# Kernel optimization log

Measured on AMD Instinct MI355X. Metric: run time of the kernel, lower is better.

## Reference

```python
import jax, jax.numpy as jnp
import numpy as np

B, LATENT, U_DIM, NUM_PROD, NUM_INJ, HID = 4096, 128, 24, 16, 8, 200
ZU = LATENT + U_DIM  # 152


def setup_inputs() -> dict:
    key = jax.random.key(0)
    ks = jax.random.split(key, 24)

    def w(k, shape, fan_in):
        return jax.random.normal(k, shape, jnp.float32) * (1.0 / np.sqrt(fan_in))

    inp = {
        "zt": jax.random.normal(ks[0], (B, LATENT), jnp.float32),
        "dt": jax.random.uniform(ks[1], (B, 1), jnp.float32),
        "ut": jax.random.uniform(ks[2], (B, U_DIM), jnp.float32),
        # trans_encoder: (latent+1) -> 200 -> 200 -> latent, ReLU between
        "We1": w(ks[3], (HID, LATENT + 1), LATENT + 1), "be1": jnp.zeros((HID,), jnp.float32),
        "We2": w(ks[4], (HID, HID), HID),               "be2": jnp.zeros((HID,), jnp.float32),
        "We3": w(ks[5], (LATENT, HID), HID),            "be3": jnp.zeros((LATENT,), jnp.float32),
        # At / Bt projections
        "WA": w(ks[6], (LATENT * LATENT, LATENT), LATENT), "bA": jnp.zeros((LATENT * LATENT,), jnp.float32),
        "WB": w(ks[7], (LATENT * U_DIM, LATENT), LATENT),  "bB": jnp.zeros((LATENT * U_DIM,), jnp.float32),
        # per-well heads, stacked over head dim h: zu(152) -> 64 -> 64 -> 2
        "Wh1": w(ks[8], (NUM_PROD, 64, ZU), ZU),  "bh1": jnp.zeros((NUM_PROD, 64), jnp.float32),
        "Wh2": w(ks[9], (NUM_PROD, 64, 64), 64),  "bh2": jnp.zeros((NUM_PROD, 64), jnp.float32),
        "Wh3": w(ks[10], (NUM_PROD, 2, 64), 64),  "bh3": jnp.zeros((NUM_PROD, 2), jnp.float32),
        # injector head: zu -> num_inj
        "Wi": w(ks[11], (NUM_INJ, ZU), ZU), "bi": jnp.zeros((NUM_INJ,), jnp.float32),
    }
    return inp


def _forward(zt, dt, ut, We1, be1, We2, be2, We3, be3, WA, bA, WB, bB,
             Wh1, bh1, Wh2, bh2, Wh3, bh3, Wi, bi):
    b = zt.shape[0]
    # encoder on [zt, dt]
    x = jnp.concatenate([zt, dt], axis=-1)                      # [B, latent+1]
    h = jax.nn.relu(x @ We1.T + be1)
    h = jax.nn.relu(h @ We2.T + be2)
    hz = h @ We3.T + be3                                        # [B, latent]
    # state transition matrices
    At = (hz @ WA.T + bA).reshape(b, LATENT, LATENT)            # [B, L, L]
    Bt = (hz @ WB.T + bB).reshape(b, LATENT, U_DIM)             # [B, L, U]
    ut_dt = ut * dt                                             # [B, U]
    zt1 = jnp.einsum('bij,bj->bi', At, zt) + jnp.einsum('biu,bu->bi', Bt, ut_dt)
    # per-well heads on zu, fused as batched GEMMs over head dim h
    zu = jnp.concatenate([zt1, ut], axis=-1)                    # [B, 152]
    g = jax.nn.relu(jnp.einsum('bz,hoz->bho', zu, Wh1) + bh1)   # [B, H, 64]
    g = jax.nn.relu(jnp.einsum('bho,hpo->bhp', g, Wh2) + bh2)   # [B, H, 64]
    wells = (jnp.einsum('bho,hpo->bhp', g, Wh3) + bh3).reshape(b, NUM_PROD * 2)
    inj = zu @ Wi.T + bi                                        # [B, num_inj]
    yt1 = jnp.concatenate([wells, inj], axis=-1)                # [B, 40]
    return zt1, yt1


def reference(zt, dt, ut, We1, be1, We2, be2, We3, be3, WA, bA, WB, bB,
              Wh1, bh1, Wh2, bh2, Wh3, bh3, Wi, bi):
    return _forward(zt, dt, ut, We1, be1, We2, be2, We3, be3, WA, bA, WB, bB,
                    Wh1, bh1, Wh2, bh2, Wh3, bh3, Wi, bi)
```

## Files before the change

### kernel.cpp

```cpp
#include <hip/hip_runtime.h>
#include <hip/hip_bf16.h>


#define NB   4096
#define LAT  128
#define UD   24
#define HIDN 200
#define ZUD  152
#define JPD  152

#define GT_OFF      0u
#define GB_OFF      2490368u
#define HZ_OFF      2509824u
#define PART_OFF    3034112u
#define PART_STRIDE 524288u
#define WH1P_OFF    7228416u
#define WH2P_OFF    7392256u
#define WH3P_OFF    7457792u

typedef __attribute__((ext_vector_type(8))) short short8_t;
typedef __attribute__((ext_vector_type(4))) float f32x4;

union FragU { short8_t s; unsigned short u[8]; };
union Frag2 { short8_t s; __hip_bfloat162 h2[4]; };

__device__ __forceinline__ unsigned short bf16_rne(float x) {
  const unsigned u = __float_as_uint(x);
  return (unsigned short)((u + 0x7FFFu + ((u >> 16) & 1u)) >> 16);
}
__device__ __forceinline__ unsigned short bf16_hi(float x) {
  return (unsigned short)(__float_as_uint(x) >> 16);
}
__device__ __forceinline__ unsigned short bf16_lo(float x) {
  const float hif = __uint_as_float(__float_as_uint(x) & 0xFFFF0000u);
  return bf16_rne(x - hif);
}

#define MFMA_BF16(A, B, C) __builtin_amdgcn_mfma_f32_16x16x32_bf16((A), (B), (C), 0, 0, 0)

__global__ __launch_bounds__(256, 5)
void prep_kernel(const float* __restrict__ WA, const float* __restrict__ bA,
                 const float* __restrict__ WB, const float* __restrict__ bB,
                 unsigned short* __restrict__ GtU, float* __restrict__ Gb,
                 const float* __restrict__ zt, const float* __restrict__ dt,
                 const float* __restrict__ We1, const float* __restrict__ be1,
                 const float* __restrict__ We2, const float* __restrict__ be2,
                 const float* __restrict__ We3, const float* __restrict__ be3,
                 float* __restrict__ hz,
                 const float* __restrict__ Wh1, const float* __restrict__ Wh2,
                 const float* __restrict__ Wh3,
                 short8_t* __restrict__ WH1P, short8_t* __restrict__ WH2P,
                 short8_t* __restrict__ WH3P) {
  __shared__ union {
    float tile32[32][132];
    struct { float xs[8][132]; float h1[8][200]; float h2[8][200]; } e;
  } sh;
  const int t = threadIdx.x;

  if (blockIdx.x < 152) {
    const int jp = blockIdx.x;
    const bool isA = (jp < LAT);
    const float* __restrict__ src = isA ? WA : WB;
    const int mul = isA ? LAT : UD;
    const int sub = isA ? jp : (jp - LAT);
    short8_t* __restrict__ G8 = (short8_t*)GtU;

    if (t < 128) {
      const float* __restrict__ bsrc = isA ? bA : bB;
      Gb[(jp << 7) + t] = bsrc[t * mul + sub];
    }

    for (int p = 0; p < 4; ++p) {
      for (int idx = t; idx < 1024; idx += 256) {
        const int i = idx >> 5, c4 = (idx & 31) << 2;
        *(float4*)(&sh.tile32[i][c4]) =
            *(const float4*)(src + (size_t)(((p << 5) + i) * mul + sub) * 128 + c4);
      }
      __syncthreads();
#pragma unroll
      for (int q = 0; q < 4; ++q) {
        const int cc  = (q << 8) + t;
        const int l   = cc & 63;
        const int spl = (cc >> 6) & 1;
        const int nloc = (cc >> 7) & 1;
        const int ksq  = (cc >> 8) & 3;
        const int n    = (p << 1) + nloc;
        const int icl  = (nloc << 4) + (l & 15);
        const int k0   = (ksq << 5) + ((l >> 4) << 3);
        FragU fr;
#pragma unroll
        for (int j = 0; j < 8; ++j) {
          const float g = sh.tile32[icl][k0 + j];
          fr.u[j] = spl ? bf16_lo(g) : bf16_hi(g);
        }
        const int c = ((((ksq << 3) + n) << 1) + spl) * 64 + l;
        G8[(size_t)jp * 4096 + c] = fr.s;
      }
      __syncthreads();
    }
    return;
  }

  if (blockIdx.x >= 664) {
    const int h = blockIdx.x - 664;
    for (int c = t; c < 2560; c += 256) {
      const int l = c & 63, spl = (c >> 6) & 1, nt = (c >> 7) & 3, ks = c >> 9;
      const int col = (nt << 4) + (l & 15);
      const int k0  = (ks << 5) + ((l >> 4) << 3);
      const float* __restrict__ wr = Wh1 + ((size_t)h * 64 + col) * ZUD;
      FragU fr;
#pragma unroll
      for (int j = 0; j < 8; ++j) {
        const int k = k0 + j;
        const float v = (k < ZUD) ? wr[k] : 0.f;
        fr.u[j] = spl ? bf16_lo(v) : bf16_hi(v);
      }
      WH1P[(size_t)h * 2560 + c] = fr.s;
    }
    for (int c = t; c < 1024; c += 256) {
      const int l = c & 63, spl = (c >> 6) & 1, nt = (c >> 7) & 3, ks = (c >> 9) & 1;
      const int col = (nt << 4) + (l & 15);
      const int k0  = (ks << 5) + ((l >> 4) << 3);
      const float* __restrict__ wr = Wh2 + ((size_t)h * 64 + col) * 64 + k0;
      FragU fr;
#pragma unroll
      for (int j = 0; j < 8; ++j) {
        const float v = wr[j];
        fr.u[j] = spl ? bf16_lo(v) : bf16_hi(v);
      }
      WH2P[(size_t)h * 1024 + c] = fr.s;
    }
    for (int c = t; c < 256; c += 256) {
      const int l = c & 63, spl = (c >> 6) & 1, ks = (c >> 7) & 1;
      const int col = l & 15;
      const int k0  = (ks << 5) + ((l >> 4) << 3);
      FragU fr;
#pragma unroll
      for (int j = 0; j < 8; ++j) {
        const float v = (col < 2) ? Wh3[((size_t)h * 2 + col) * 64 + k0 + j] : 0.f;
        fr.u[j] = spl ? bf16_lo(v) : bf16_hi(v);
      }
      WH3P[(size_t)h * 256 + c] = fr.s;
    }
    return;
  }

  const int b0 = (blockIdx.x - 152) * 8;

  for (int idx = t; idx < 8 * 129; idx += 256) {
    const int r = idx / 129, c = idx - r * 129;
    sh.e.xs[r][c] = (c < LAT) ? zt[(size_t)(b0 + r) * LAT + c] : dt[b0 + r];
  }
  __syncthreads();

  if (t < HIDN) {
    const float* __restrict__ w = We1 + t * 129;
    float acc[8];
    const float bias = be1[t];
#pragma unroll
    for (int r = 0; r < 8; ++r) acc[r] = bias;
    for (int c = 0; c < 128; c += 4) {
      const float w0 = w[c], w1 = w[c + 1], w2 = w[c + 2], w3 = w[c + 3];
#pragma unroll
      for (int r = 0; r < 8; ++r) {
        const float4 xv = *(const float4*)(&sh.e.xs[r][c]);
        acc[r] += xv.x * w0 + xv.y * w1 + xv.z * w2 + xv.w * w3;
      }
    }
    const float wl = w[128];
#pragma unroll
    for (int r = 0; r < 8; ++r) sh.e.h1[r][t] = fmaxf(fmaf(sh.e.xs[r][128], wl, acc[r]), 0.f);
  }
  __syncthreads();

  if (t < HIDN) {
    const float* __restrict__ w = We2 + t * HIDN;
    float acc[8];
    const float bias = be2[t];
#pragma unroll
    for (int r = 0; r < 8; ++r) acc[r] = bias;
    for (int c = 0; c < HIDN; c += 4) {
      const float4 wv = *(const float4*)(w + c);
#pragma unroll
      for (int r = 0; r < 8; ++r) {
        const float4 hv = *(const float4*)(&sh.e.h1[r][c]);
        acc[r] += hv.x * wv.x + hv.y * wv.y + hv.z * wv.z + hv.w * wv.w;
      }
    }
#pragma unroll
    for (int r = 0; r < 8; ++r) sh.e.h2[r][t] = fmaxf(acc[r], 0.f);
  }
  __syncthreads();

  if (t < LAT) {
    const float* __restrict__ w = We3 + t * HIDN;
    float acc[8];
    const float bias = be3[t];
#pragma unroll
    for (int r = 0; r < 8; ++r) acc[r] = bias;
    for (int c = 0; c < HIDN; c += 4) {
      const float4 wv = *(const float4*)(w + c);
#pragma unroll
      for (int r = 0; r < 8; ++r) {
        const float4 hv = *(const float4*)(&sh.e.h2[r][c]);
        acc[r] += hv.x * wv.x + hv.y * wv.y + hv.z * wv.z + hv.w * wv.w;
      }
    }
#pragma unroll
    for (int r = 0; r < 8; ++r) hz[(size_t)(b0 + r) * LAT + t] = acc[r];
  }
}

#define GBODY(JP, B00, B01, B10, B11, NJP)                                      \
  {                                                                             \
    const int jp_ = (JP);                                                       \
    const float w0_ = wtile[(rw << 5) + lr][jp_];                               \
    const float w1_ = wtile[(rw << 5) + 16 + lr][jp_];                          \
    Frag2 p0_, p1_;                                                             \
    _Pragma("unroll")                                                           \
    for (int jq = 0; jq < 4; ++jq) {                                            \
      p0_.h2[jq] = __float22bfloat162_rn(                                       \
          make_float2(w0_ * hzr0[2 * jq], w0_ * hzr0[2 * jq + 1]));             \
      p1_.h2[jq] = __float22bfloat162_rn(                                       \
          make_float2(w1_ * hzr1[2 * jq], w1_ * hzr1[2 * jq + 1]));             \
    }                                                                           \
    acc00 = MFMA_BF16(p0_.s, B00, acc00);                                       \
    acc00 = MFMA_BF16(p0_.s, B01, acc00);                                       \
    acc01 = MFMA_BF16(p0_.s, B10, acc01);                                       \
    acc01 = MFMA_BF16(p0_.s, B11, acc01);                                       \
    acc10 = MFMA_BF16(p1_.s, B00, acc10);                                       \
    acc10 = MFMA_BF16(p1_.s, B01, acc10);                                       \
    acc11 = MFMA_BF16(p1_.s, B10, acc11);                                       \
    acc11 = MFMA_BF16(p1_.s, B11, acc11);                                       \
    const size_t nb_ = (size_t)(NJP) * 4096;                                    \
    B00 = G8[nb_ + c00]; B01 = G8[nb_ + c01];                                   \
    B10 = G8[nb_ + c10]; B11 = G8[nb_ + c11];                                   \
  }

__global__ __launch_bounds__(512, 4)
void gemm_mfma_kernel(const float* __restrict__ zt, const float* __restrict__ dt,
                      const float* __restrict__ ut,
                      const unsigned short* __restrict__ GtU,
                      const float* __restrict__ Gb,
                      const float* __restrict__ hz, float* __restrict__ part) {
  __shared__ float wtile[64][156];
  const int t  = threadIdx.x;
  const int l  = t & 63;
  const int w  = t >> 6;
  const int rw = w & 1, cw = w >> 1;
  const int bid   = blockIdx.x;
  const int combo = bid & 7;
  const int ks    = combo & 3;
  const int jph   = combo >> 2;
  const int b0    = (bid >> 3) << 6;
  const int lr  = l & 15, lg = l >> 4;
  const int j0  = jph * 76;

  for (int idx = t; idx < 2048; idx += 512) {
    const int r = idx >> 5, c4 = (idx & 31) << 2;
    *(float4*)(&wtile[r][c4]) = *(const float4*)(zt + (((size_t)(b0 + r)) << 7) + c4);
  }
  for (int idx = t; idx < 384; idx += 512) {
    const int r = idx / 6, u4 = (idx - r * 6) << 2;
    float4 v = *(const float4*)(ut + (size_t)(b0 + r) * UD + u4);
    const float s = dt[b0 + r];
    v.x *= s; v.y *= s; v.z *= s; v.w *= s;
    *(float4*)(&wtile[r][LAT + u4]) = v;
  }
  __syncthreads();

  const int kk = (ks << 5) + (lg << 3);
  float hzr0[8], hzr1[8];
  {
    const float* __restrict__ hp0 = hz + (((size_t)(b0 + (rw << 5) + lr)) << 7) + kk;
    const float* __restrict__ hp1 = hz + (((size_t)(b0 + (rw << 5) + 16 + lr)) << 7) + kk;
    const float4 a0 = *(const float4*)hp0, b0v = *(const float4*)(hp0 + 4);
    const float4 a1 = *(const float4*)hp1, b1v = *(const float4*)(hp1 + 4);
    hzr0[0]=a0.x; hzr0[1]=a0.y; hzr0[2]=a0.z; hzr0[3]=a0.w;
    hzr0[4]=b0v.x; hzr0[5]=b0v.y; hzr0[6]=b0v.z; hzr0[7]=b0v.w;
    hzr1[0]=a1.x; hzr1[1]=a1.y; hzr1[2]=a1.z; hzr1[3]=a1.w;
    hzr1[4]=b1v.x; hzr1[5]=b1v.y; hzr1[6]=b1v.z; hzr1[7]=b1v.w;
  }

  const short8_t* __restrict__ G8 = (const short8_t*)GtU;
  const int n0 = (cw << 1), n1 = (cw << 1) + 1;
  const int c00 = ((((ks << 3) + n0) << 1) + 0) * 64 + l;
  const int c01 = ((((ks << 3) + n0) << 1) + 1) * 64 + l;
  const int c10 = ((((ks << 3) + n1) << 1) + 0) * 64 + l;
  const int c11 = ((((ks << 3) + n1) << 1) + 1) * 64 + l;

  f32x4 acc00 = {0.f,0.f,0.f,0.f}, acc01 = {0.f,0.f,0.f,0.f};
  f32x4 acc10 = {0.f,0.f,0.f,0.f}, acc11 = {0.f,0.f,0.f,0.f};

  short8_t A0 = G8[(size_t)(j0+0)*4096 + c00], A1 = G8[(size_t)(j0+0)*4096 + c01],
           A2 = G8[(size_t)(j0+0)*4096 + c10], A3 = G8[(size_t)(j0+0)*4096 + c11];
  short8_t Bv0 = G8[(size_t)(j0+1)*4096 + c00], Bv1 = G8[(size_t)(j0+1)*4096 + c01],
           Bv2 = G8[(size_t)(j0+1)*4096 + c10], Bv3 = G8[(size_t)(j0+1)*4096 + c11];
  short8_t C0 = G8[(size_t)(j0+2)*4096 + c00], C1 = G8[(size_t)(j0+2)*4096 + c01],
           C2 = G8[(size_t)(j0+2)*4096 + c10], C3 = G8[(size_t)(j0+2)*4096 + c11];
  short8_t D0 = G8[(size_t)(j0+3)*4096 + c00], D1 = G8[(size_t)(j0+3)*4096 + c01],
           D2 = G8[(size_t)(j0+3)*4096 + c10], D3 = G8[(size_t)(j0+3)*4096 + c11];

  const int jend = j0 + 76;
  for (int jp = j0; jp < jend; jp += 4) {
    const int n4 = (jp + 4 < jend) ? jp + 4 : jend - 1;
    const int n5 = (jp + 5 < jend) ? jp + 5 : jend - 1;
    const int n6 = (jp + 6 < jend) ? jp + 6 : jend - 1;
    const int n7 = (jp + 7 < jend) ? jp + 7 : jend - 1;
    GBODY(jp + 0, A0, A1, A2, A3, n4);
    GBODY(jp + 1, Bv0, Bv1, Bv2, Bv3, n5);
    GBODY(jp + 2, C0, C1, C2, C3, n6);
    GBODY(jp + 3, D0, D1, D2, D3, n7);
  }

  {
    const int jb0 = combo * 19;
    for (int jp = jb0; jp < jb0 + 19; ++jp) {
      const float gb0 = Gb[(jp << 7) + (cw << 5) + lr];
      const float gb1 = Gb[(jp << 7) + (cw << 5) + 16 + lr];
#pragma unroll
      for (int r = 0; r < 4; ++r) {
        const float wv0 = wtile[(rw << 5) + (lg << 2) + r][jp];
        const float wv1 = wtile[(rw << 5) + 16 + (lg << 2) + r][jp];
        acc00[r] += wv0 * gb0; acc01[r] += wv0 * gb1;
        acc10[r] += wv1 * gb0; acc11[r] += wv1 * gb1;
      }
    }
  }

  float* __restrict__ dst = part + (size_t)combo * PART_STRIDE + (((size_t)b0) << 7);
  const int colb = (cw << 5) + lr;
#pragma unroll
  for (int r = 0; r < 4; ++r) {
    const int row0 = (rw << 5) + (lg << 2) + r;
    const int row1 = row0 + 16;
    dst[((size_t)row0 << 7) + colb]      = acc00[r];
    dst[((size_t)row0 << 7) + colb + 16] = acc01[r];
    dst[((size_t)row1 << 7) + colb]      = acc10[r];
    dst[((size_t)row1 << 7) + colb + 16] = acc11[r];
  }
}

__global__ __launch_bounds__(512, 4)
void heads_kernel(const float* __restrict__ ut, const float* __restrict__ part,
                  const short8_t* __restrict__ WH1P, const float* __restrict__ bh1,
                  const short8_t* __restrict__ WH2P, const float* __restrict__ bh2,
                  const short8_t* __restrict__ WH3P, const float* __restrict__ bh3,
                  const float* __restrict__ Wi, const float* __restrict__ bi,
                  float* __restrict__ out) {
  __shared__ float    zuf[64][156];
  __shared__ short8_t g1a[1024];
  __shared__ short8_t g2a[1024];
  const int t  = threadIdx.x;
  const int l  = t & 63;
  const int w  = t >> 6;
  const int wm = w >> 1, wn = w & 1;
  const int mb = blockIdx.x >> 2;
  const int hg = blockIdx.x & 3;
  const int b0 = mb << 6;
  float* __restrict__ zt1_out = out;
  float* __restrict__ yt1_out = out + (size_t)NB * LAT;

  for (int idx = t; idx < 2048; idx += 512) {
    const int r = idx >> 5, c4 = (idx & 31) << 2;
    const size_t off = (((size_t)(b0 + r)) << 7) + c4;
    float4 s = *(const float4*)(part + off);
#pragma unroll
    for (int q = 1; q < 8; ++q) {
      const float4 v = *(const float4*)(part + (size_t)q * PART_STRIDE + off);
      s.x += v.x; s.y += v.y; s.z += v.z; s.w += v.w;
    }
    *(float4*)(&zuf[r][c4]) = s;
    if (hg == 0) *(float4*)(zt1_out + off) = s;
  }
  for (int idx = t; idx < 384; idx += 512) {
    const int r = idx / 6, u4 = (idx - r * 6) << 2;
    *(float4*)(&zuf[r][LAT + u4]) = *(const float4*)(ut + (size_t)(b0 + r) * UD + u4);
  }
  __syncthreads();

  short8_t Ahi[5], Alo[5];
  {
    const int arow = (wm << 4) + (l & 15);
#pragma unroll
    for (int ks = 0; ks < 5; ++ks) {
      const int k0 = (ks << 5) + ((l >> 4) << 3);
      FragU fh, fl;
      if (k0 < ZUD) {
        const float4 va = *(const float4*)(&zuf[arow][k0]);
        const float4 vb = *(const float4*)(&zuf[arow][k0 + 4]);
        const float vv[8] = {va.x, va.y, va.z, va.w, vb.x, vb.y, vb.z, vb.w};
#pragma unroll
        for (int j = 0; j < 8; ++j) { fh.u[j] = bf16_hi(vv[j]); fl.u[j] = bf16_lo(vv[j]); }
      } else {
#pragma unroll
        for (int j = 0; j < 8; ++j) { fh.u[j] = 0; fl.u[j] = 0; }
      }
      Ahi[ks] = fh.s; Alo[ks] = fl.s;
    }
  }

  unsigned short* __restrict__ g1s = (unsigned short*)g1a;
  unsigned short* __restrict__ g2s = (unsigned short*)g2a;
  const int lq = l >> 4;

  for (int hc = 0; hc < 4; ++hc) {
    const int hh = (hg << 2) + hc;

    const short8_t* __restrict__ W1 = WH1P + (size_t)hh * 2560;
    short8_t b1h[5][2], b1l[5][2];
#pragma unroll
    for (int ks = 0; ks < 5; ++ks)
#pragma unroll
      for (int nt = 0; nt < 2; ++nt) {
        const int ntg = (wn << 1) + nt;
        b1h[ks][nt] = W1[(((ks << 2) + ntg) * 2 + 0) * 64 + l];
        b1l[ks][nt] = W1[(((ks << 2) + ntg) * 2 + 1) * 64 + l];
      }
    f32x4 a1[2] = {{0.f,0.f,0.f,0.f},{0.f,0.f,0.f,0.f}};
#pragma unroll
    for (int ks = 0; ks < 5; ++ks)
#pragma unroll
      for (int nt = 0; nt < 2; ++nt) {
        a1[nt] = MFMA_BF16(Ahi[ks], b1h[ks][nt], a1[nt]);
        a1[nt] = MFMA_BF16(Alo[ks], b1h[ks][nt], a1[nt]);
        a1[nt] = MFMA_BF16(Ahi[ks], b1l[ks][nt], a1[nt]);
      }
#pragma unroll
    for (int nt = 0; nt < 2; ++nt) {
      const int C = (wn << 5) + (nt << 4) + (l & 15);
      const float bv = bh1[(hh << 6) + C];
      const int chunkbase = (((wm << 1) + (C >> 5)) << 1);
#pragma unroll
      for (int r = 0; r < 4; ++r) {
        const float v = fmaxf(a1[nt][r] + bv, 0.f);
        const int lane2 = ((lq << 2) + r) | ((((C >> 3) & 3)) << 4);
        g1s[(((chunkbase + 0) * 64 + lane2) << 3) + (C & 7)] = bf16_hi(v);
        g1s[(((chunkbase + 1) * 64 + lane2) << 3) + (C & 7)] = bf16_lo(v);
      }
    }
    __syncthreads();

    const short8_t* __restrict__ W2 = WH2P + (size_t)hh * 1024;
    short8_t A2h[2], A2l[2];
#pragma unroll
    for (int ks = 0; ks < 2; ++ks) {
      A2h[ks] = g1a[(((wm << 1) + ks) * 2 + 0) * 64 + l];
      A2l[ks] = g1a[(((wm << 1) + ks) * 2 + 1) * 64 + l];
    }
    f32x4 a2[2] = {{0.f,0.f,0.f,0.f},{0.f,0.f,0.f,0.f}};
#pragma unroll
    for (int ks = 0; ks < 2; ++ks)
#pragma unroll
      for (int nt = 0; nt < 2; ++nt) {
        const int ntg = (wn << 1) + nt;
        const short8_t bh = W2[(((ks << 2) + ntg) * 2 + 0) * 64 + l];
        const short8_t bl = W2[(((ks << 2) + ntg) * 2 + 1) * 64 + l];
        a2[nt] = MFMA_BF16(A2h[ks], bh, a2[nt]);
        a2[nt] = MFMA_BF16(A2l[ks], bh, a2[nt]);
        a2[nt] = MFMA_BF16(A2h[ks], bl, a2[nt]);
      }
#pragma unroll
    for (int nt = 0; nt < 2; ++nt) {
      const int C = (wn << 5) + (nt << 4) + (l & 15);
      const float bv = bh2[(hh << 6) + C];
      const int chunkbase = (((wm << 1) + (C >> 5)) << 1);
#pragma unroll
      for (int r = 0; r < 4; ++r) {
        const float v = fmaxf(a2[nt][r] + bv, 0.f);
        const int lane2 = ((lq << 2) + r) | ((((C >> 3) & 3)) << 4);
        g2s[(((chunkbase + 0) * 64 + lane2) << 3) + (C & 7)] = bf16_hi(v);
        g2s[(((chunkbase + 1) * 64 + lane2) << 3) + (C & 7)] = bf16_lo(v);
      }
    }
    __syncthreads();

    if (wn == 0) {
      const short8_t* __restrict__ W3 = WH3P + (size_t)hh * 256;
      f32x4 a3 = {0.f,0.f,0.f,0.f};
#pragma unroll
      for (int ks = 0; ks < 2; ++ks) {
        const short8_t Ah = g2a[(((wm << 1) + ks) * 2 + 0) * 64 + l];
        const short8_t Al = g2a[(((wm << 1) + ks) * 2 + 1) * 64 + l];
        const short8_t bh = W3[((ks << 1) + 0) * 64 + l];
        const short8_t bl = W3[((ks << 1) + 1) * 64 + l];
        a3 = MFMA_BF16(Ah, bh, a3);
        a3 = MFMA_BF16(Al, bh, a3);
        a3 = MFMA_BF16(Ah, bl, a3);
      }
      if ((l & 15) < 2) {
        const int col = l & 15;
        const float bv = bh3[(hh << 1) + col];
#pragma unroll
        for (int r = 0; r < 4; ++r) {
          const int R = (wm << 4) + (lq << 2) + r;
          yt1_out[(size_t)(b0 + R) * 40 + (hh << 1) + col] = a3[r] + bv;
        }
      }
    }
  }

  if (hg == 3) {
    const int r  = t >> 3, io = t & 7;
    const float4* __restrict__ wrow = (const float4*)(Wi + (size_t)io * ZUD);
    const float4* __restrict__ zr   = (const float4*)(&zuf[r][0]);
    float a0 = 0, a1 = 0, a2 = 0, a3 = 0;
#pragma unroll
    for (int cc = 0; cc < 38; ++cc) {
      const float4 wv = wrow[cc];
      const float4 zv = zr[cc];
      a0 = fmaf(wv.x, zv.x, a0); a1 = fmaf(wv.y, zv.y, a1);
      a2 = fmaf(wv.z, zv.z, a2); a3 = fmaf(wv.w, zv.w, a3);
    }
    yt1_out[(size_t)(b0 + r) * 40 + 32 + io] = a0 + a1 + a2 + a3 + bi[io];
  }
}

extern "C" void kernel_launch(void* const* d_in, const int* in_sizes, int n_in,
                              void* d_out, int out_size, void* d_ws, size_t ws_size,
                              hipStream_t stream) {
  const float* zt  = (const float*)d_in[0];
  const float* dt  = (const float*)d_in[1];
  const float* ut  = (const float*)d_in[2];
  const float* We1 = (const float*)d_in[3];
  const float* be1 = (const float*)d_in[4];
  const float* We2 = (const float*)d_in[5];
  const float* be2 = (const float*)d_in[6];
  const float* We3 = (const float*)d_in[7];
  const float* be3 = (const float*)d_in[8];
  const float* WA  = (const float*)d_in[9];
  const float* bA  = (const float*)d_in[10];
  const float* WB  = (const float*)d_in[11];
  const float* bB  = (const float*)d_in[12];
  const float* Wh1 = (const float*)d_in[13];
  const float* bh1 = (const float*)d_in[14];
  const float* Wh2 = (const float*)d_in[15];
  const float* bh2 = (const float*)d_in[16];
  const float* Wh3 = (const float*)d_in[17];
  const float* bh3 = (const float*)d_in[18];
  const float* Wi  = (const float*)d_in[19];
  const float* bi  = (const float*)d_in[20];

  float* ws = (float*)d_ws;
  unsigned short* GtU = (unsigned short*)(ws + GT_OFF);
  float* Gb   = ws + GB_OFF;
  float* hz   = ws + HZ_OFF;
  float* part = ws + PART_OFF;
  short8_t* WH1P = (short8_t*)(ws + WH1P_OFF);
  short8_t* WH2P = (short8_t*)(ws + WH2P_OFF);
  short8_t* WH3P = (short8_t*)(ws + WH3P_OFF);
  float* out  = (float*)d_out;

  hipLaunchKernelGGL(prep_kernel, dim3(152 + NB / 8 + 16), dim3(256), 0, stream,
                     WA, bA, WB, bB, GtU, Gb,
                     zt, dt, We1, be1, We2, be2, We3, be3, hz,
                     Wh1, Wh2, Wh3, WH1P, WH2P, WH3P);
  hipLaunchKernelGGL(gemm_mfma_kernel, dim3(512), dim3(512), 0, stream,
                     zt, dt, ut, GtU, Gb, hz, part);
  hipLaunchKernelGGL(heads_kernel, dim3(256), dim3(512), 0, stream,
                     ut, part, WH1P, bh1, WH2P, bh2, WH3P, bh3, Wi, bi, out);
}
```

Baseline: 234.7 us.

## Run encoder MLP on split-bf16 MFMA and grid-stride weight packing in prep

```diff
diff --git a/kernel.cpp b/kernel.cpp
--- a/kernel.cpp
+++ b/kernel.cpp
@@ -8,6 +8,9 @@
 #define HIDN 200
 #define ZUD  152
 #define JPD  152
+
+#define ENC_NB  256
+#define PACK_NB 512
 
 #define GT_OFF      0u
 #define GB_OFF      2490368u
@@ -35,10 +38,22 @@
   const float hif = __uint_as_float(__float_as_uint(x) & 0xFFFF0000u);
   return bf16_rne(x - hif);
 }
+__device__ __forceinline__ void build_hilo8(const float* vv, short8_t& hi, short8_t& lo) {
+  FragU fh; Frag2 fl;
+#pragma unroll
+  for (int j = 0; j < 8; ++j) fh.u[j] = bf16_hi(vv[j]);
+#pragma unroll
+  for (int j = 0; j < 4; ++j) {
+    const float d0 = vv[2*j]   - __uint_as_float(__float_as_uint(vv[2*j])   & 0xFFFF0000u);
+    const float d1 = vv[2*j+1] - __uint_as_float(__float_as_uint(vv[2*j+1]) & 0xFFFF0000u);
+    fl.h2[j] = __float22bfloat162_rn(make_float2(d0, d1));
+  }
+  hi = fh.s; lo = fl.s;
+}
 
 #define MFMA_BF16(A, B, C) __builtin_amdgcn_mfma_f32_16x16x32_bf16((A), (B), (C), 0, 0, 0)
 
-__global__ __launch_bounds__(256, 5)
+__global__ __launch_bounds__(512, 4)
 void prep_kernel(const float* __restrict__ WA, const float* __restrict__ bA,
                  const float* __restrict__ WB, const float* __restrict__ bB,
                  unsigned short* __restrict__ GtU, float* __restrict__ Gb,
@@ -51,163 +66,221 @@
                  const float* __restrict__ Wh3,
                  short8_t* __restrict__ WH1P, short8_t* __restrict__ WH2P,
                  short8_t* __restrict__ WH3P) {
-  __shared__ union {
-    float tile32[32][132];
-    struct { float xs[8][132]; float h1[8][200]; float h2[8][200]; } e;
-  } sh;
+  __shared__ float bufA[16][260];
+  __shared__ float bufB[16][260];
   const int t = threadIdx.x;
 
-  if (blockIdx.x < 152) {
-    const int jp = blockIdx.x;
-    const bool isA = (jp < LAT);
-    const float* __restrict__ src = isA ? WA : WB;
-    const int mul = isA ? LAT : UD;
-    const int sub = isA ? jp : (jp - LAT);
-    short8_t* __restrict__ G8 = (short8_t*)GtU;
-
-    if (t < 128) {
-      const float* __restrict__ bsrc = isA ? bA : bB;
-      Gb[(jp << 7) + t] = bsrc[t * mul + sub];
-    }
-
-    for (int p = 0; p < 4; ++p) {
-      for (int idx = t; idx < 1024; idx += 256) {
-        const int i = idx >> 5, c4 = (idx & 31) << 2;
-        *(float4*)(&sh.tile32[i][c4]) =
-            *(const float4*)(src + (size_t)(((p << 5) + i) * mul + sub) * 128 + c4);
-      }
-      __syncthreads();
-#pragma unroll
-      for (int q = 0; q < 4; ++q) {
-        const int cc  = (q << 8) + t;
-        const int l   = cc & 63;
-        const int spl = (cc >> 6) & 1;
-        const int nloc = (cc >> 7) & 1;
-        const int ksq  = (cc >> 8) & 3;
-        const int n    = (p << 1) + nloc;
-        const int icl  = (nloc << 4) + (l & 15);
-        const int k0   = (ksq << 5) + ((l >> 4) << 3);
-        FragU fr;
-#pragma unroll
-        for (int j = 0; j < 8; ++j) {
-          const float g = sh.tile32[icl][k0 + j];
-          fr.u[j] = spl ? bf16_lo(g) : bf16_hi(g);
+  if (blockIdx.x < ENC_NB) {
+    const int b0 = blockIdx.x << 4;
+    for (int idx = t; idx < 16 * 160; idx += 512) {
+      const int r = idx / 160, c = idx - r * 160;
+      float v = 0.f;
+      if (c < LAT) v = zt[(size_t)(b0 + r) * LAT + c];
+      else if (c == LAT) v = dt[b0 + r];
+      bufA[r][c] = v;
+    }
+    if (t < 256) {
+      bufB[t >> 4][208 + (t & 15)] = 0.f;
+    }
+    __syncthreads();
+
+    const int w  = t >> 6;
+    const int l  = t & 63;
+    const int lr = l & 15, lg = l >> 4;
+    const int kbase = lg << 3;
+
+    {
+      short8_t Ah[5], Al[5];
+#pragma unroll
+      for (int kf = 0; kf < 5; ++kf) {
+        float vv[8];
+        const float* ap = &bufA[lr][(kf << 5) + kbase];
+        *(float4*)(vv)     = *(const float4*)(ap);
+        *(float4*)(vv + 4) = *(const float4*)(ap + 4);
+        build_hilo8(vv, Ah[kf], Al[kf]);
+      }
+#pragma unroll
+      for (int tt = 0; tt < 2; ++tt) {
+        const int nt = w + (tt << 3);
+        if (nt > 12) break;
+        const int col = (nt << 4) + lr;
+        f32x4 acc = {0.f, 0.f, 0.f, 0.f};
+#pragma unroll
+        for (int kf = 0; kf < 5; ++kf) {
+          const int k0 = (kf << 5) + kbase;
+          float vv[8];
+          if (col < HIDN) {
+            const float* wp = We1 + (size_t)col * 129 + k0;
+#pragma unroll
+            for (int j = 0; j < 8; ++j) vv[j] = (k0 + j < 129) ? wp[j] : 0.f;
+          } else {
+#pragma unroll
+            for (int j = 0; j < 8; ++j) vv[j] = 0.f;
+          }
+          short8_t Bh, Bl;
+          build_hilo8(vv, Bh, Bl);
+          acc = MFMA_BF16(Ah[kf], Bh, acc);
+          acc = MFMA_BF16(Al[kf], Bh, acc);
+          acc = MFMA_BF16(Ah[kf], Bl, acc);
         }
-        const int c = ((((ksq << 3) + n) << 1) + spl) * 64 + l;
-        G8[(size_t)jp * 4096 + c] = fr.s;
-      }
-      __syncthreads();
+        const float bv = (col < HIDN) ? be1[col] : 0.f;
+#pragma unroll
+        for (int r = 0; r < 4; ++r)
+          bufB[(lg << 2) + r][col] = fmaxf(acc[r] + bv, 0.f);
+      }
+    }
+    __syncthreads();
+
+    {
+      short8_t Ah[7], Al[7];
+#pragma unroll
+      for (int kf = 0; kf < 7; ++kf) {
+        float vv[8];
+        const float* ap = &bufB[lr][(kf << 5) + kbase];
+        *(float4*)(vv)     = *(const float4*)(ap);
+        *(float4*)(vv + 4) = *(const float4*)(ap + 4);
+        build_hilo8(vv, Ah[kf], Al[kf]);
+      }
+#pragma unroll
+      for (int tt = 0; tt < 2; ++tt) {
+        const int nt = w + (tt << 3);
+        if (nt > 13) break;
+        const int col = (nt << 4) + lr;
+        f32x4 acc = {0.f, 0.f, 0.f, 0.f};
+#pragma unroll
+        for (int kf = 0; kf < 7; ++kf) {
+          const int k0 = (kf << 5) + kbase;
+          float vv[8];
+          if (col < HIDN && k0 < HIDN) {
+            const float* wp = We2 + (size_t)col * HIDN + k0;
+            *(float4*)(vv)     = *(const float4*)(wp);
+            *(float4*)(vv + 4) = *(const float4*)(wp + 4);
+          } else {
+#pragma unroll
+            for (int j = 0; j < 8; ++j) vv[j] = 0.f;
+          }
+          short8_t Bh, Bl;
+          build_hilo8(vv, Bh, Bl);
+          acc = MFMA_BF16(Ah[kf], Bh, acc);
+          acc = MFMA_BF16(Al[kf], Bh, acc);
+          acc = MFMA_BF16(Ah[kf], Bl, acc);
+        }
+        const float bv = (col < HIDN) ? be2[col] : 0.f;
+#pragma unroll
+        for (int r = 0; r < 4; ++r)
+          bufA[(lg << 2) + r][col] = fmaxf(acc[r] + bv, 0.f);
+      }
+    }
+    __syncthreads();
+
+    {
+      short8_t Ah[7], Al[7];
+#pragma unroll
+      for (int kf = 0; kf < 7; ++kf) {
+        float vv[8];
+        const float* ap = &bufA[lr][(kf << 5) + kbase];
+        *(float4*)(vv)     = *(const float4*)(ap);
+        *(float4*)(vv + 4) = *(const float4*)(ap + 4);
+        build_hilo8(vv, Ah[kf], Al[kf]);
+      }
+      const int col = (w << 4) + lr;
+      f32x4 acc = {0.f, 0.f, 0.f, 0.f};
+#pragma unroll
+      for (int kf = 0; kf < 7; ++kf) {
+        const int k0 = (kf << 5) + kbase;
+        float vv[8];
+        if (k0 < HIDN) {
+          const float* wp = We3 + (size_t)col * HIDN + k0;
+          *(float4*)(vv)     = *(const float4*)(wp);
+          *(float4*)(vv + 4) = *(const float4*)(wp + 4);
+        } else {
+#pragma unroll
+          for (int j = 0; j < 8; ++j) vv[j] = 0.f;
+        }
+        short8_t Bh, Bl;
+        build_hilo8(vv, Bh, Bl);
+        acc = MFMA_BF16(Ah[kf], Bh, acc);
+        acc = MFMA_BF16(Al[kf], Bh, acc);
+        acc = MFMA_BF16(Ah[kf], Bl, acc);
+      }
+      const float bv = be3[col];
+#pragma unroll
+      for (int r = 0; r < 4; ++r)
+        hz[(size_t)(b0 + (lg << 2) + r) * LAT + col] = acc[r] + bv;
     }
     return;
   }
 
-  if (blockIdx.x >= 664) {
-    const int h = blockIdx.x - 664;
-    for (int c = t; c < 2560; c += 256) {
-      const int l = c & 63, spl = (c >> 6) & 1, nt = (c >> 7) & 3, ks = c >> 9;
-      const int col = (nt << 4) + (l & 15);
-      const int k0  = (ks << 5) + ((l >> 4) << 3);
-      const float* __restrict__ wr = Wh1 + ((size_t)h * 64 + col) * ZUD;
-      FragU fr;
-#pragma unroll
-      for (int j = 0; j < 8; ++j) {
-        const int k = k0 + j;
-        const float v = (k < ZUD) ? wr[k] : 0.f;
-        fr.u[j] = spl ? bf16_lo(v) : bf16_hi(v);
-      }
-      WH1P[(size_t)h * 2560 + c] = fr.s;
-    }
-    for (int c = t; c < 1024; c += 256) {
-      const int l = c & 63, spl = (c >> 6) & 1, nt = (c >> 7) & 3, ks = (c >> 9) & 1;
-      const int col = (nt << 4) + (l & 15);
-      const int k0  = (ks << 5) + ((l >> 4) << 3);
-      const float* __restrict__ wr = Wh2 + ((size_t)h * 64 + col) * 64 + k0;
-      FragU fr;
-#pragma unroll
-      for (int j = 0; j < 8; ++j) {
-        const float v = wr[j];
-        fr.u[j] = spl ? bf16_lo(v) : bf16_hi(v);
-      }
-      WH2P[(size_t)h * 1024 + c] = fr.s;
-    }
-    for (int c = t; c < 256; c += 256) {
-      const int l = c & 63, spl = (c >> 6) & 1, ks = (c >> 7) & 1;
-      const int col = l & 15;
-      const int k0  = (ks << 5) + ((l >> 4) << 3);
-      FragU fr;
-#pragma unroll
-      for (int j = 0; j < 8; ++j) {
-        const float v = (col < 2) ? Wh3[((size_t)h * 2 + col) * 64 + k0 + j] : 0.f;
-        fr.u[j] = spl ? bf16_lo(v) : bf16_hi(v);
-      }
-      WH3P[(size_t)h * 256 + c] = fr.s;
-    }
-    return;
-  }
-
-  const int b0 = (blockIdx.x - 152) * 8;
-
-  for (int idx = t; idx < 8 * 129; idx += 256) {
-    const int r = idx / 129, c = idx - r * 129;
-    sh.e.xs[r][c] = (c < LAT) ? zt[(size_t)(b0 + r) * LAT + c] : dt[b0 + r];
-  }
-  __syncthreads();
-
-  if (t < HIDN) {
-    const float* __restrict__ w = We1 + t * 129;
-    float acc[8];
-    const float bias = be1[t];
-#pragma unroll
-    for (int r = 0; r < 8; ++r) acc[r] = bias;
-    for (int c = 0; c < 128; c += 4) {
-      const float w0 = w[c], w1 = w[c + 1], w2 = w[c + 2], w3 = w[c + 3];
-#pragma unroll
-      for (int r = 0; r < 8; ++r) {
-        const float4 xv = *(const float4*)(&sh.e.xs[r][c]);
-        acc[r] += xv.x * w0 + xv.y * w1 + xv.z * w2 + xv.w * w3;
-      }
-    }
-    const float wl = w[128];
-#pragma unroll
-    for (int r = 0; r < 8; ++r) sh.e.h1[r][t] = fmaxf(fmaf(sh.e.xs[r][128], wl, acc[r]), 0.f);
-  }
-  __syncthreads();
-
-  if (t < HIDN) {
-    const float* __restrict__ w = We2 + t * HIDN;
-    float acc[8];
-    const float bias = be2[t];
-#pragma unroll
-    for (int r = 0; r < 8; ++r) acc[r] = bias;
-    for (int c = 0; c < HIDN; c += 4) {
-      const float4 wv = *(const float4*)(w + c);
-#pragma unroll
-      for (int r = 0; r < 8; ++r) {
-        const float4 hv = *(const float4*)(&sh.e.h1[r][c]);
-        acc[r] += hv.x * wv.x + hv.y * wv.y + hv.z * wv.z + hv.w * wv.w;
-      }
-    }
-#pragma unroll
-    for (int r = 0; r < 8; ++r) sh.e.h2[r][t] = fmaxf(acc[r], 0.f);
-  }
-  __syncthreads();
-
-  if (t < LAT) {
-    const float* __restrict__ w = We3 + t * HIDN;
-    float acc[8];
-    const float bias = be3[t];
-#pragma unroll
-    for (int r = 0; r < 8; ++r) acc[r] = bias;
-    for (int c = 0; c < HIDN; c += 4) {
-      const float4 wv = *(const float4*)(w + c);
-#pragma unroll
-      for (int r = 0; r < 8; ++r) {
-        const float4 hv = *(const float4*)(&sh.e.h2[r][c]);
-        acc[r] += hv.x * wv.x + hv.y * wv.y + hv.z * wv.z + hv.w * wv.w;
-      }
-    }
-#pragma unroll
-    for (int r = 0; r < 8; ++r) hz[(size_t)(b0 + r) * LAT + t] = acc[r];
+  const int tid = (blockIdx.x - ENC_NB) * 512 + t;
+  const int NT  = PACK_NB * 512;
+
+  short8_t* __restrict__ G8 = (short8_t*)GtU;
+  for (int g = tid; g < JPD * 4096; g += NT) {
+    const int jp = g >> 12, c = g & 4095;
+    const int l = c & 63, spl = (c >> 6) & 1, n = (c >> 7) & 7, ksq = (c >> 10) & 3;
+    const int icol = (n << 4) + (l & 15);
+    const int k0 = (ksq << 5) + ((l >> 4) << 3);
+    const float* __restrict__ src = (jp < LAT)
+        ? WA + ((size_t)(icol * LAT + jp)) * 128 + k0
+        : WB + ((size_t)(icol * UD + (jp - LAT))) * 128 + k0;
+    float vv[8];
+    *(float4*)(vv)     = *(const float4*)(src);
+    *(float4*)(vv + 4) = *(const float4*)(src + 4);
+    FragU fr;
+    if (spl == 0) {
+#pragma unroll
+      for (int j = 0; j < 8; ++j) fr.u[j] = bf16_hi(vv[j]);
+    } else {
+#pragma unroll
+      for (int j = 0; j < 8; ++j) fr.u[j] = bf16_lo(vv[j]);
+    }
+    G8[g] = fr.s;
+  }
+  for (int g = tid; g < JPD * LAT; g += NT) {
+    const int jp = g >> 7, i = g & 127;
+    Gb[g] = (jp < LAT) ? bA[i * LAT + jp] : bB[i * UD + (jp - LAT)];
+  }
+  for (int g = tid; g < 16 * 2560; g += NT) {
+    const int h = g / 2560, c = g - h * 2560;
+    const int l = c & 63, spl = (c >> 6) & 1, nt = (c >> 7) & 3, ks = c >> 9;
+    const int col = (nt << 4) + (l & 15);
+    const int k0 = (ks << 5) + ((l >> 4) << 3);
+    const float* __restrict__ wr = Wh1 + ((size_t)h * 64 + col) * ZUD;
+    FragU fr;
+#pragma unroll
+    for (int j = 0; j < 8; ++j) {
+      const int k = k0 + j;
+      const float v = (k < ZUD) ? wr[k] : 0.f;
+      fr.u[j] = spl ? bf16_lo(v) : bf16_hi(v);
+    }
+    WH1P[g] = fr.s;
+  }
+  for (int g = tid; g < 16 * 1024; g += NT) {
+    const int h = g >> 10, c = g & 1023;
+    const int l = c & 63, spl = (c >> 6) & 1, nt = (c >> 7) & 3, ks = (c >> 9) & 1;
+    const int col = (nt << 4) + (l & 15);
+    const int k0 = (ks << 5) + ((l >> 4) << 3);
+    const float* __restrict__ wr = Wh2 + ((size_t)h * 64 + col) * 64 + k0;
+    FragU fr;
+#pragma unroll
+    for (int j = 0; j < 8; ++j) {
+      const float v = wr[j];
+      fr.u[j] = spl ? bf16_lo(v) : bf16_hi(v);
+    }
+    WH2P[g] = fr.s;
+  }
+  for (int g = tid; g < 16 * 256; g += NT) {
+    const int h = g >> 8, c = g & 255;
+    const int l = c & 63, spl = (c >> 6) & 1, ks = (c >> 7) & 1;
+    const int col = l & 15;
+    const int k0 = (ks << 5) + ((l >> 4) << 3);
+    FragU fr;
+#pragma unroll
+    for (int j = 0; j < 8; ++j) {
+      const float v = (col < 2) ? Wh3[((size_t)h * 2 + col) * 64 + k0 + j] : 0.f;
+      fr.u[j] = spl ? bf16_lo(v) : bf16_hi(v);
+    }
+    WH3P[g] = fr.s;
   }
 }
 
@@ -551,7 +624,7 @@
   short8_t* WH3P = (short8_t*)(ws + WH3P_OFF);
   float* out  = (float*)d_out;
 
-  hipLaunchKernelGGL(prep_kernel, dim3(152 + NB / 8 + 16), dim3(256), 0, stream,
+  hipLaunchKernelGGL(prep_kernel, dim3(ENC_NB + PACK_NB), dim3(512), 0, stream,
                      WA, bA, WB, bB, GtU, Gb,
                      zt, dt, We1, be1, We2, be2, We3, be3, hz,
                      Wh1, Wh2, Wh3, WH1P, WH2P, WH3P);
```

New measurement: 197.8 us. -15.7%, faster.
